# Kernel tuning notes

Measured on AMD Instinct MI355X. Metric: run time of the kernel, lower is better.

## Reference

```python
import jax, jax.numpy as jnp
import numpy as np

EPS = 1e-4

@jax.custom_vjp
def binarize(x):
    # BinaryConnectDeterministic: sign with sign(0)=+1
    return jnp.where(x >= 0, 1.0, -1.0).astype(x.dtype)

def _bin_fwd(x):
    return binarize(x), x

def _bin_bwd(x, g):
    # straight-through estimator, clipped to |x| <= 1
    return (g * (jnp.abs(x) <= 1).astype(g.dtype),)

binarize.defvjp(_bin_fwd, _bin_bwd)

def ap2(x):
    # approximate power-of-2: sign(x) * 2^round(log2|x|); grad is 0 a.e. (round/sign)
    a = jnp.maximum(jnp.abs(x), 1e-38)
    return jnp.sign(x) * jnp.exp2(jnp.round(jnp.log2(a)))

def shift_bn(x, gamma, beta, axes):
    # shift-based batch norm (BNN paper): var approximated via centered*AP2(centered),
    # inverse std and gamma replaced by their AP2 approximations. Training-mode batch stats.
    mean = jnp.mean(x, axis=axes, keepdims=True)
    c = x - mean
    var = jnp.mean(c * ap2(c), axis=axes, keepdims=True)
    xhat = c * ap2(1.0 / jnp.sqrt(var + EPS))
    shape = [1] * x.ndim
    shape[1] = x.shape[1]
    return ap2(gamma.reshape(shape)) * xhat + beta.reshape(shape)

def conv_bin(x, w, b):
    y = jax.lax.conv_general_dilated(x, binarize(w), (1, 1), [(1, 1), (1, 1)],
                                     dimension_numbers=('NCHW', 'OIHW', 'NCHW'))
    return y + b[None, :, None, None]

def maxpool3s2(x):
    return jax.lax.reduce_window(x, -jnp.inf, jax.lax.max,
                                 (1, 1, 3, 3), (1, 1, 2, 2), 'VALID')


def setup_inputs() -> dict:
    key = jax.random.key(0)
    ks = jax.random.split(key, 8)
    B, NU = 2048, 2048
    inp = {
        'x': jax.random.normal(ks[0], (B, 784), jnp.float32),
        'conv1_w': jax.random.normal(ks[1], (32, 1, 3, 3), jnp.float32) * 0.1,
        'conv1_b': jnp.zeros((32,), jnp.float32),
        'g1': jnp.ones((32,), jnp.float32), 'b1': jnp.zeros((32,), jnp.float32),
        'conv2_w': jax.random.normal(ks[2], (64, 32, 3, 3), jnp.float32) * 0.1,
        'conv2_b': jnp.zeros((64,), jnp.float32),
        'g2': jnp.ones((64,), jnp.float32), 'b2': jnp.zeros((64,), jnp.float32),
        'lin3_w': jax.random.normal(ks[3], (NU, 10816), jnp.float32) * 0.02,
        'lin3_b': jnp.zeros((NU,), jnp.float32),
        'g3': jnp.ones((NU,), jnp.float32), 'b3': jnp.zeros((NU,), jnp.float32),
        'lin4_w': jax.random.normal(ks[4], (10, NU), jnp.float32) * 0.02,
        'lin4_b': jnp.zeros((10,), jnp.float32),
    }
    return inp


def reference(x, conv1_w, conv1_b, g1, b1, conv2_w, conv2_b, g2, b2,
              lin3_w, lin3_b, g3, b3, lin4_w, lin4_b):
    h = x.reshape(-1, 1, 28, 28)
    h = jax.nn.relu(conv_bin(h, conv1_w, conv1_b))
    h = shift_bn(h, g1, b1, axes=(0, 2, 3))
    h = binarize(h)
    h = jax.nn.relu(conv_bin(h, conv2_w, conv2_b))
    h = maxpool3s2(h)                       # [B,64,13,13]
    h = shift_bn(h, g2, b2, axes=(0, 2, 3))
    h = binarize(h)
    h = h.reshape(h.shape[0], -1)           # [B,10816]
    h = jax.nn.relu(h @ binarize(lin3_w).T + lin3_b)
    h = shift_bn(h, g3, b3, axes=(0,))
    h = binarize(h)
    return h @ binarize(lin4_w).T + lin4_b  # [B,10] (no norm4/logsoftmax in forward)
```

## Files before the change

### kernel.cpp

```cpp
#include <hip/hip_runtime.h>

#define BB 2048
#define IMG 784
#define HWD 28
#define C1 32
#define C2 64
#define PP 169
#define PD 13
#define F3 10816
#define N3 2048
#define K4W 32
#define NOUT 10
#define CONV 27
#define PADW 30
#define OCCHUNK 8
#define IMGC 29
#define SCRP 740

typedef unsigned long long u64;
typedef int v4i __attribute__((ext_vector_type(4)));
typedef int v16i __attribute__((ext_vector_type(16)));

#define GLOAD16(gp, lp) __builtin_amdgcn_global_load_lds( \
    (__attribute__((address_space(1))) void*)(gp),        \
    (__attribute__((address_space(3))) void*)(lp), 16, 0, 0)

__device__ __forceinline__ float ap2mag(float c) {
    unsigned int a = __float_as_uint(c) & 0x7fffffffu;
    unsigned int e = (a >> 23) + ((a & 0x7fffffu) > 0x3504f3u);
    return __uint_as_float(e << 23);
}
__device__ __forceinline__ float ap2sgn(float g) {
    unsigned int u = __float_as_uint(g);
    unsigned int a = u & 0x7fffffffu;
    if (a == 0) return 0.f;
    unsigned int e = (a >> 23) + ((a & 0x7fffffu) > 0x3504f3u);
    return __uint_as_float((u & 0x80000000u) | (e << 23));
}

__global__ __launch_bounds__(256) void stage0(const float* __restrict__ x,
                                              const float* __restrict__ w1, const float* __restrict__ cb1,
                                              float* __restrict__ part1, float* __restrict__ w1b,
                                              const float* __restrict__ w2, char* __restrict__ w2i8,
                                              const float* __restrict__ w3, char* __restrict__ wp3i,
                                              const float* __restrict__ w4, u64* __restrict__ wp4) {
    __shared__ float xs[30 * PADW];
    __shared__ float red[4 * C1];
    int n = blockIdx.x, tid = threadIdx.x;
    int lane = tid & 63, wv = tid >> 6;
    {
        int idx = n * 256 + tid;
        int nthr = gridDim.x * 256;
        int total = (N3 * F3) / 4;
        for (int t = idx; t < total; t += nthr) {
            float4 wv4 = *(const float4*)(w3 + (size_t)t * 4);
            unsigned int w = (wv4.x >= 0.f ? 0x01u : 0xffu)
                           | (wv4.y >= 0.f ? 0x01u : 0xffu) << 8
                           | (wv4.z >= 0.f ? 0x01u : 0xffu) << 16
                           | (wv4.w >= 0.f ? 0x01u : 0xffu) << 24;
            *(unsigned int*)(wp3i + (size_t)t * 4) = w;
        }
    }
    if (n == 0) {
        for (int i = tid; i < C1 * 9; i += 256) w1b[i] = (w1[i] >= 0.f) ? 1.f : -1.f;
    } else if (n == 1) {
        for (int i = tid; i < 2 * 9 * 64 * 16; i += 256) {
            int hf = i / 9216;
            int r = i - hf * 9216;
            int t = r >> 10;
            int l = (r >> 4) & 63;
            int j = i & 15;
            int oc = hf * 32 + (l & 31);
            int ic = ((l >> 5) << 4) + j;
            w2i8[i] = (w2[oc * 288 + ic * 9 + t] >= 0.f) ? (char)1 : (char)(-1);
        }
    } else if (n == 2) {
        for (int w = wv; w < NOUT * K4W; w += 4) {
            int o = w / K4W, j = w % K4W;
            float wvl = w4[o * N3 + j * 64 + lane];
            u64 mask = __ballot(wvl >= 0.f);
            if (lane == 0) wp4[w] = mask;
        }
    }
    for (int i = tid; i < 30 * PADW; i += 256) {
        int r = i / PADW - 1, c = i % PADW - 1;
        float v = 0.f;
        if (r >= 0 && r < HWD && c >= 0 && c < HWD) v = x[n * IMG + r * HWD + c];
        xs[i] = v;
    }
    __syncthreads();
    bool act = tid < 196;
    int r = tid / 7, c0 = (tid % 7) * 4;
    float win[18];
#pragma unroll
    for (int k = 0; k < 18; k++) win[k] = 0.f;
    if (act) {
#pragma unroll
        for (int ry = 0; ry < 3; ry++)
#pragma unroll
            for (int cx = 0; cx < 6; cx++)
                win[ry * 6 + cx] = xs[(r + ry) * PADW + c0 + cx];
    }
#pragma unroll
    for (int ch = 0; ch < C1; ch++) {
        float a = 0.f;
        if (act) {
            float k0 = (w1[ch * 9 + 0] >= 0.f) ? 1.f : -1.f, k1 = (w1[ch * 9 + 1] >= 0.f) ? 1.f : -1.f;
            float k2 = (w1[ch * 9 + 2] >= 0.f) ? 1.f : -1.f, k3 = (w1[ch * 9 + 3] >= 0.f) ? 1.f : -1.f;
            float k4 = (w1[ch * 9 + 4] >= 0.f) ? 1.f : -1.f, k5 = (w1[ch * 9 + 5] >= 0.f) ? 1.f : -1.f;
            float k6 = (w1[ch * 9 + 6] >= 0.f) ? 1.f : -1.f, k7 = (w1[ch * 9 + 7] >= 0.f) ? 1.f : -1.f;
            float k8 = (w1[ch * 9 + 8] >= 0.f) ? 1.f : -1.f;
            float b = cb1[ch];
#pragma unroll
            for (int px = 0; px < 4; px++) {
                float s = win[px] * k0 + win[px + 1] * k1 + win[px + 2] * k2
                        + win[6 + px] * k3 + win[7 + px] * k4 + win[8 + px] * k5
                        + win[12 + px] * k6 + win[13 + px] * k7 + win[14 + px] * k8;
                a += fmaxf(s + b, 0.f);
            }
        }
        for (int off = 32; off; off >>= 1) a += __shfl_down(a, off);
        if (lane == 0) red[wv * C1 + ch] = a;
    }
    __syncthreads();
    if (tid < C1) part1[n * C1 + tid] = red[tid] + red[C1 + tid] + red[2 * C1 + tid] + red[3 * C1 + tid];
}

__global__ __launch_bounds__(256) void conv1_var(const float* __restrict__ x,
                            const float* __restrict__ w1b,
                            const float* __restrict__ cb1, const float* __restrict__ mean1,
                            float* __restrict__ part) {
    __shared__ float xs[30 * PADW];
    __shared__ float red[4 * C1];
    int n = blockIdx.x, tid = threadIdx.x;
    for (int i = tid; i < 30 * PADW; i += 256) {
        int r = i / PADW - 1, c = i % PADW - 1;
        float v = 0.f;
        if (r >= 0 && r < HWD && c >= 0 && c < HWD) v = x[n * IMG + r * HWD + c];
        xs[i] = v;
    }
    __syncthreads();
    bool act = tid < 196;
    int r = tid / 7, c0 = (tid % 7) * 4;
    float win[18];
#pragma unroll
    for (int k = 0; k < 18; k++) win[k] = 0.f;
    if (act) {
#pragma unroll
        for (int ry = 0; ry < 3; ry++)
#pragma unroll
            for (int cx = 0; cx < 6; cx++)
                win[ry * 6 + cx] = xs[(r + ry) * PADW + c0 + cx];
    }
    int lane = tid & 63, wv = tid >> 6;
#pragma unroll
    for (int ch = 0; ch < C1; ch++) {
        float a = 0.f;
        if (act) {
            float k0 = w1b[ch * 9 + 0], k1 = w1b[ch * 9 + 1], k2 = w1b[ch * 9 + 2];
            float k3 = w1b[ch * 9 + 3], k4 = w1b[ch * 9 + 4], k5 = w1b[ch * 9 + 5];
            float k6 = w1b[ch * 9 + 6], k7 = w1b[ch * 9 + 7], k8 = w1b[ch * 9 + 8];
            float b = cb1[ch], m = mean1[ch];
#pragma unroll
            for (int px = 0; px < 4; px++) {
                float s = win[px] * k0 + win[px + 1] * k1 + win[px + 2] * k2
                        + win[6 + px] * k3 + win[7 + px] * k4 + win[8 + px] * k5
                        + win[12 + px] * k6 + win[13 + px] * k7 + win[14 + px] * k8;
                float v = fmaxf(s + b, 0.f);
                float c = v - m;
                a += fabsf(c) * ap2mag(c);
            }
        }
        for (int off = 32; off; off >>= 1) a += __shfl_down(a, off);
        if (lane == 0) red[wv * C1 + ch] = a;
    }
    __syncthreads();
    if (tid < C1) part[n * C1 + tid] = red[tid] + red[C1 + tid] + red[2 * C1 + tid] + red[3 * C1 + tid];
}

__global__ __launch_bounds__(256) void conv1_pack(const float* __restrict__ x,
                           const float* __restrict__ w1b,
                           const float* __restrict__ cb1, const float* __restrict__ mean1,
                           const float* __restrict__ scale1, const float* __restrict__ beta1,
                           unsigned int* __restrict__ s1p) {
    __shared__ float xs[30 * PADW];
    int n = blockIdx.x, tid = threadIdx.x;
    for (int i = tid; i < 30 * PADW; i += 256) {
        int r = i / PADW - 1, c = i % PADW - 1;
        float v = 0.f;
        if (r >= 0 && r < HWD && c >= 0 && c < HWD) v = x[n * IMG + r * HWD + c];
        xs[i] = v;
    }
    __syncthreads();
    if (tid >= 196) return;
    int r = tid / 7, c0 = (tid % 7) * 4;
    float win[18];
#pragma unroll
    for (int ry = 0; ry < 3; ry++)
#pragma unroll
        for (int cx = 0; cx < 6; cx++)
            win[ry * 6 + cx] = xs[(r + ry) * PADW + c0 + cx];
    unsigned int bits0 = 0, bits1 = 0, bits2 = 0, bits3 = 0;
#pragma unroll
    for (int ch = 0; ch < C1; ch++) {
        float k0 = w1b[ch * 9 + 0], k1 = w1b[ch * 9 + 1], k2 = w1b[ch * 9 + 2];
        float k3 = w1b[ch * 9 + 3], k4 = w1b[ch * 9 + 4], k5 = w1b[ch * 9 + 5];
        float k6 = w1b[ch * 9 + 6], k7 = w1b[ch * 9 + 7], k8 = w1b[ch * 9 + 8];
        float b = cb1[ch], m = mean1[ch], sc = scale1[ch], bt = beta1[ch];
#pragma unroll
        for (int px = 0; px < 4; px++) {
            float s = win[px] * k0 + win[px + 1] * k1 + win[px + 2] * k2
                    + win[6 + px] * k3 + win[7 + px] * k4 + win[8 + px] * k5
                    + win[12 + px] * k6 + win[13 + px] * k7 + win[14 + px] * k8;
            float v = fmaxf(s + b, 0.f);
            float val = sc * (v - m) + bt;
            unsigned int bit = (val >= 0.f ? 1u : 0u) << ch;
            if (px == 0) bits0 |= bit;
            else if (px == 1) bits1 |= bit;
            else if (px == 2) bits2 |= bit;
            else bits3 |= bit;
        }
    }
    uint4 w4v = make_uint4(bits0, bits1, bits2, bits3);
    *reinterpret_cast<uint4*>(&s1p[n * IMG + r * HWD + c0]) = w4v;
}

__global__ __launch_bounds__(256) void conv2pool(const unsigned int* __restrict__ s1p,
                                                 const char* __restrict__ w2i8,
                                                 const float* __restrict__ cb2,
                                                 short* __restrict__ p2i,
                                                 float* __restrict__ part2) {
    __shared__ char img[IMGC * IMGC * 32];
    __shared__ short scr[32 * SCRP];
    __shared__ float psum[OCCHUNK * PP];
    __shared__ float pm[C2];
    int n = blockIdx.x, tid = threadIdx.x;
    int lane = tid & 63, wv = tid >> 6;
    for (int i = tid; i < IMGC * IMGC; i += 256) {
        int r = i / IMGC, c = i - r * IMGC;
        unsigned int w = 0u;
        if (r >= 1 && c >= 1) w = s1p[n * IMG + (r - 1) * HWD + (c - 1)];
        unsigned int d[8];
        if (r == 0 || c == 0) {
#pragma unroll
            for (int e = 0; e < 8; e++) d[e] = 0u;
        } else {
#pragma unroll
            for (int e = 0; e < 8; e++) {
                unsigned int nib = (w >> (4 * e)) & 0xFu;
                unsigned int t = (nib & 1u) | ((nib & 2u) << 7) | ((nib & 4u) << 14) | ((nib & 8u) << 21);
                d[e] = 0xFFFFFFFFu - t * 0xFEu;
            }
        }
        *(uint4*)&img[i * 32] = make_uint4(d[0], d[1], d[2], d[3]);
        *(uint4*)&img[i * 32 + 16] = make_uint4(d[4], d[5], d[6], d[7]);
    }
    __syncthreads();
    int hh = lane >> 5;
    int l31 = lane & 31;
    for (int hf = 0; hf < 2; hf++) {
        v4i bf[9];
#pragma unroll
        for (int t = 0; t < 9; t++)
            bf[t] = *(const v4i*)(w2i8 + (hf * 9 + t) * 1024 + lane * 16);
#pragma unroll
        for (int j = 0; j < 3; j++) {
            int mtA = wv + 8 * j, mtB = mtA + 4;
            int pA = mtA * 32 + l31; if (pA > 728) pA = 728;
            int pB = mtB * 32 + l31; if (pB > 728) pB = 728;
            int yA = pA / 27, xA = pA - yA * 27;
            int yB = pB / 27, xB = pB - yB * 27;
            int aA = (yA * IMGC + xA) * 32 + hh * 16;
            int aB = (yB * IMGC + xB) * 32 + hh * 16;
            v16i accA = {0,0,0,0,0,0,0,0,0,0,0,0,0,0,0,0};
            v16i accB = {0,0,0,0,0,0,0,0,0,0,0,0,0,0,0,0};
#pragma unroll
            for (int ky = 0; ky < 3; ky++)
#pragma unroll
                for (int kx = 0; kx < 3; kx++) {
                    v4i fA = *(const v4i*)&img[aA + (ky * IMGC + kx) * 32];
                    v4i fB = *(const v4i*)&img[aB + (ky * IMGC + kx) * 32];
                    accA = __builtin_amdgcn_mfma_i32_32x32x32_i8(fA, bf[ky * 3 + kx], accA, 0, 0, 0);
                    accB = __builtin_amdgcn_mfma_i32_32x32x32_i8(fB, bf[ky * 3 + kx], accB, 0, 0, 0);
                }
            short* sr = &scr[l31 * SCRP];
#pragma unroll
            for (int g = 0; g < 4; g++) {
                short4 sA;
                sA.x = (short)accA[4 * g + 0]; sA.y = (short)accA[4 * g + 1];
                sA.z = (short)accA[4 * g + 2]; sA.w = (short)accA[4 * g + 3];
                *(short4*)&sr[mtA * 32 + g * 8 + 4 * hh] = sA;
            }
            if (mtB < 23) {
#pragma unroll
                for (int g = 0; g < 4; g++) {
                    short4 sB;
                    sB.x = (short)accB[4 * g + 0]; sB.y = (short)accB[4 * g + 1];
                    sB.z = (short)accB[4 * g + 2]; sB.w = (short)accB[4 * g + 3];
                    *(short4*)&sr[mtB * 32 + g * 8 + 4 * hh] = sB;
                }
            }
        }
        __syncthreads();
        for (int base = 0; base < 32; base += OCCHUNK) {
            for (int q = tid; q < OCCHUNK * PP; q += 256) {
                int ol = q / PP, pix = q - ol * PP;
                int py = pix / PD, px = pix - py * PD;
                const short* rr = &scr[(base + ol) * SCRP + (2 * py) * CONV + 2 * px];
                int m0 = max(max((int)rr[0], (int)rr[1]), (int)rr[2]);
                int m1 = max(max((int)rr[CONV], (int)rr[CONV + 1]), (int)rr[CONV + 2]);
                int m2 = max(max((int)rr[2 * CONV], (int)rr[2 * CONV + 1]), (int)rr[2 * CONV + 2]);
                int val = max(max(m0, m1), m2);
                int oc = hf * 32 + base + ol;
                p2i[n * F3 + oc * PP + pix] = (short)val;
                psum[q] = fmaxf((float)val + cb2[oc], 0.f);
            }
            __syncthreads();
            for (int ol = wv; ol < OCCHUNK; ol += 4) {
                float a = 0.f;
                for (int pp = lane; pp < PP; pp += 64) a += psum[ol * PP + pp];
                for (int off = 32; off; off >>= 1) a += __shfl_down(a, off);
                if (lane == 0) pm[hf * 32 + base + ol] = a;
            }
            __syncthreads();
        }
    }
    if (tid < C2) part2[n * C2 + tid] = pm[tid];
}

__global__ __launch_bounds__(256) void p2_var(const short* __restrict__ p2i,
                         const float* __restrict__ cb2,
                         const float* __restrict__ mean2, float* __restrict__ part) {
    int n = blockIdx.x, tid = threadIdx.x, lane = tid & 63, wv = tid >> 6;
    const short* rowb = p2i + (size_t)n * F3;
    __shared__ float red[C2];
#pragma unroll
    for (int i = 0; i < 16; i++) {
        int ch = wv * 16 + i;
        const short* row = rowb + ch * PP;
        float b = cb2[ch];
        float m = mean2[ch];
        float a = 0.f;
        for (int p = lane; p < PP; p += 64) {
            float v = fmaxf((float)row[p] + b, 0.f);
            float c = v - m;
            a += fabsf(c) * ap2mag(c);
        }
        for (int off = 32; off; off >>= 1) a += __shfl_down(a, off);
        if (lane == 0) red[ch] = a;
    }
    __syncthreads();
    if (tid < C2) part[n * C2 + tid] = red[tid];
}

__global__ __launch_bounds__(256) void reduce_stats(const float* __restrict__ part, int nch, int nblk,
                             const float* __restrict__ g, float* __restrict__ outv,
                             int mode, double count) {
    int ch = blockIdx.x, tid = threadIdx.x;
    double a = 0.0;
    for (int i = tid; i < nblk; i += 256) a += (double)part[(size_t)i * nch + ch];
    __shared__ double red[4];
    for (int off = 32; off; off >>= 1) a += __shfl_down(a, off);
    int lane = tid & 63, wv = tid >> 6;
    if (lane == 0) red[wv] = a;
    __syncthreads();
    if (tid == 0) {
        double s = red[0] + red[1] + red[2] + red[3];
        if (mode == 0) {
            outv[ch] = (float)(s / count);
        } else {
            float var = (float)(s / count);
            float inv = 1.0f / sqrtf(var + 1e-4f);
            outv[ch] = ap2sgn(g[ch]) * ap2mag(inv);
        }
    }
}

__global__ __launch_bounds__(256) void p2_packi8(const short* __restrict__ p2i, const float* __restrict__ cb2,
                        const float* __restrict__ mean2, const float* __restrict__ scale2,
                        const float* __restrict__ beta2, char* __restrict__ hp3i) {
    int idx = blockIdx.x * 256 + threadIdx.x;
    int nthr = gridDim.x * 256;
    int total = (BB * F3) / 4;
    for (int t = idx; t < total; t += nthr) {
        int base = t * 4;
        int f0 = base % F3;
        unsigned int w = 0;
#pragma unroll
        for (int e = 0; e < 4; e++) {
            int f = f0 + e;
            int oc = f / PP;
            float v = fmaxf((float)p2i[base + e] + cb2[oc], 0.f);
            float val = scale2[oc] * (v - mean2[oc]) + beta2[oc];
            w |= (val >= 0.f ? 0x01u : 0xffu) << (8 * e);
        }
        *(unsigned int*)(hp3i + base) = w;
    }
}

__global__ __launch_bounds__(256) void lin3_mfma(const char* __restrict__ hp3i,
                                                 const char* __restrict__ wp3i,
                                                 const float* __restrict__ b3l,
                                                 float* __restrict__ h3,
                                                 float* __restrict__ h3T,
                                                 float* __restrict__ part3) {
    __shared__ v4i aL[3][1024];
    __shared__ v4i bL[3][512];
    __shared__ float csr[4][32];
    int tid = threadIdx.x;
    int lane = tid & 63, wv = tid >> 6;
    int wr = wv >> 1, wc = wv & 1;
    int m0 = blockIdx.y * 128, n0 = blockIdx.x * 64;
    int loff = (lane & 15) * F3 + (lane >> 4) * 16;
    const char* gA0 = hp3i + (size_t)(m0 + wv * 16) * F3 + loff;
    const char* gA1 = gA0 + (size_t)64 * F3;
    const char* gB0 = wp3i + (size_t)(n0 + wv * 16) * F3 + loff;
    char* ldsA = (char*)&aL[0][0];
    char* ldsB = (char*)&bL[0][0];
    int sA = wv * 1024;
    v4i acc[4][2];
#pragma unroll
    for (int i = 0; i < 4; i++)
#pragma unroll
        for (int j = 0; j < 2; j++) acc[i][j] = (v4i){0, 0, 0, 0};

    auto stage = [&](int c) {
        int b = c % 3;
        const char* pA0 = gA0 + (size_t)c * 128;
        const char* pA1 = gA1 + (size_t)c * 128;
        const char* pB0 = gB0 + (size_t)c * 128;
        char* dA = ldsA + b * 16384 + sA;
        char* dB = ldsB + b * 8192 + sA;
        GLOAD16(pA0, dA);
        GLOAD16(pA1, dA + 4096);
        GLOAD16(pA0 + 64, dA + 8192);
        GLOAD16(pA1 + 64, dA + 12288);
        GLOAD16(pB0, dB);
        GLOAD16(pB0 + 64, dB + 4096);
    };
    auto compute = [&](int c, int nks) {
        int cur = c % 3;
        const v4i* aC = &aL[cur][0];
        const v4i* bC = &bL[cur][0];
        for (int ks = 0; ks < nks; ++ks) {
            v4i af[4], bf[2];
#pragma unroll
            for (int i = 0; i < 4; i++) af[i] = aC[ks * 512 + (wr * 4 + i) * 64 + lane];
#pragma unroll
            for (int j = 0; j < 2; j++) bf[j] = bC[ks * 256 + (wc * 2 + j) * 64 + lane];
            __builtin_amdgcn_s_setprio(1);
#pragma unroll
            for (int i = 0; i < 4; i++)
#pragma unroll
                for (int j = 0; j < 2; j++)
                    acc[i][j] = __builtin_amdgcn_mfma_i32_16x16x64_i8(af[i], bf[j], acc[i][j], 0, 0, 0);
            __builtin_amdgcn_s_setprio(0);
        }
    };

    stage(0);
    stage(1);
    asm volatile("s_waitcnt vmcnt(6)" ::: "memory");
    __builtin_amdgcn_s_barrier();
    __builtin_amdgcn_sched_barrier(0);
    for (int c = 0; c < 83; ++c) {
        stage(c + 2);
        compute(c, 2);
        asm volatile("s_waitcnt vmcnt(6)" ::: "memory");
        __builtin_amdgcn_s_barrier();
        __builtin_amdgcn_sched_barrier(0);
    }
    compute(83, 2);
    asm volatile("s_waitcnt vmcnt(0)" ::: "memory");
    __builtin_amdgcn_s_barrier();
    __builtin_amdgcn_sched_barrier(0);
    compute(84, 1);

    int q = lane >> 4, m16 = lane & 15;
    float cs[2] = {0.f, 0.f};
#pragma unroll
    for (int j = 0; j < 2; j++) {
        int col = n0 + wc * 32 + j * 16 + m16;
        float bias = b3l[col];
#pragma unroll
        for (int i = 0; i < 4; i++) {
            int rowb = m0 + wr * 64 + i * 16 + q * 4;
            float4 t4;
#pragma unroll
            for (int rg = 0; rg < 4; rg++) {
                float v = fmaxf((float)acc[i][j][rg] + bias, 0.f);
                h3[(size_t)(rowb + rg) * N3 + col] = v;
                ((float*)&t4)[rg] = v;
                cs[j] += v;
            }
            *(float4*)&h3T[(size_t)col * BB + rowb] = t4;
        }
    }
#pragma unroll
    for (int j = 0; j < 2; j++) {
        cs[j] += __shfl_xor(cs[j], 16);
        cs[j] += __shfl_xor(cs[j], 32);
        if (lane < 16) csr[wv][j * 16 + m16] = cs[j];
    }
    __syncthreads();
    if (tid < 64) {
        int wcc = tid >> 5, cc = tid & 31;
        part3[(size_t)blockIdx.y * N3 + n0 + tid] = csr[wcc][cc] + csr[2 + wcc][cc];
    }
}

__global__ __launch_bounds__(256) void h3_finish(const float* __restrict__ h3T,
                                                 const float* __restrict__ part3,
                                                 const float* __restrict__ g3,
                                                 float* __restrict__ mean3, float* __restrict__ scale3) {
    int nn = blockIdx.x, tid = threadIdx.x;
    __shared__ float msh;
    __shared__ double redd[4];
    if (tid < 64) {
        float a = (tid < 16) ? part3[(size_t)tid * N3 + nn] : 0.f;
        for (int off = 8; off; off >>= 1) a += __shfl_down(a, off);
        if (tid == 0) { float m = a / (float)BB; mean3[nn] = m; msh = m; }
    }
    __syncthreads();
    float m = msh;
    float acc = 0.f;
#pragma unroll
    for (int q = 0; q < 8; q++) {
        float v = h3T[(size_t)nn * BB + q * 256 + tid];
        float c = v - m;
        acc += fabsf(c) * ap2mag(c);
    }
    double a = (double)acc;
    for (int off = 32; off; off >>= 1) a += __shfl_down(a, off);
    int lane = tid & 63, wv = tid >> 6;
    if (lane == 0) redd[wv] = a;
    __syncthreads();
    if (tid == 0) {
        float var = (float)((redd[0] + redd[1] + redd[2] + redd[3]) / (double)BB);
        float inv = 1.0f / sqrtf(var + 1e-4f);
        scale3[nn] = ap2sgn(g3[nn]) * ap2mag(inv);
    }
}

__global__ __launch_bounds__(256) void h4_out(const float* __restrict__ h3,
                                              const float* __restrict__ mean3, const float* __restrict__ scale3,
                                              const float* __restrict__ bt3,
                                              const u64* __restrict__ wp4, const float* __restrict__ b4,
                                              float* __restrict__ out) {
    __shared__ u64 hb[K4W];
    __shared__ u64 wsh[NOUT * 33];
    int m = blockIdx.x, tid = threadIdx.x, lane = tid & 63, wv = tid >> 6;
    for (int i = tid; i < NOUT * K4W; i += 256) wsh[(i / K4W) * 33 + (i % K4W)] = wp4[i];
#pragma unroll
    for (int q = 0; q < 8; q++) {
        int j = wv * 8 + q;
        int f = j * 64 + lane;
        float v = h3[(size_t)m * N3 + f];
        float val = scale3[f] * (v - mean3[f]) + bt3[f];
        u64 mask = __ballot(val >= 0.f);
        if (lane == 0) hb[j] = mask;
    }
    __syncthreads();
    if (tid < NOUT) {
        int c = 0;
#pragma unroll
        for (int k = 0; k < K4W; k++) c += (int)__popcll(hb[k] ^ wsh[tid * 33 + k]);
        out[m * NOUT + tid] = (float)(N3 - 2 * c) + b4[tid];
    }
}

extern "C" void kernel_launch(void* const* d_in, const int* in_sizes, int n_in,
                              void* d_out, int out_size, void* d_ws, size_t ws_size,
                              hipStream_t stream) {
    const float* x   = (const float*)d_in[0];
    const float* w1  = (const float*)d_in[1];
    const float* cb1 = (const float*)d_in[2];
    const float* g1  = (const float*)d_in[3];
    const float* bt1 = (const float*)d_in[4];
    const float* w2  = (const float*)d_in[5];
    const float* cb2 = (const float*)d_in[6];
    const float* g2  = (const float*)d_in[7];
    const float* bt2 = (const float*)d_in[8];
    const float* w3  = (const float*)d_in[9];
    const float* b3l = (const float*)d_in[10];
    const float* g3  = (const float*)d_in[11];
    const float* bt3 = (const float*)d_in[12];
    const float* w4  = (const float*)d_in[13];
    const float* b4l = (const float*)d_in[14];
    float* out = (float*)d_out;

    char* base = (char*)d_ws;
    size_t off = 0;
    auto carve = [&](size_t bytes) { char* p = base + off; off = (off + bytes + 255) & ~(size_t)255; return p; };
    char* bufA = carve((size_t)BB * C2 * PP * 2);
    char* bufB = carve((size_t)BB * F3);
    char* bufC = carve((size_t)N3 * F3);
    short* p2i         = (short*)bufA;
    float* h3          = (float*)bufA;
    float* h3T         = (float*)(bufA + (size_t)BB * N3 * 4);
    char* hp3i         = bufB;
    unsigned int* s1p  = (unsigned int*)bufB;
    char* wp3i         = bufC;
    u64* wp4           = (u64*)carve((size_t)NOUT * K4W * 8);
    char* w2i8         = (char*)carve((size_t)2 * 9 * 64 * 16);
    float* w1b         = (float*)carve((size_t)C1 * 9 * 4);
    float* part1       = (float*)carve((size_t)BB * C1 * 4);
    float* part2       = (float*)carve((size_t)BB * C2 * 4);
    float* part3       = (float*)carve((size_t)16 * N3 * 4);
    float* fstats      = (float*)carve((size_t)(32 + 32 + 64 + 64 + 2048 + 2048) * 4);
    float* mean1 = fstats;          float* scale1 = fstats + 32;
    float* mean2 = fstats + 64;     float* scale2 = fstats + 128;
    float* mean3 = fstats + 192;    float* scale3 = fstats + 2240;

    stage0<<<BB, 256, 0, stream>>>(x, w1, cb1, part1, w1b, w2, w2i8, w3, wp3i, w4, wp4);
    reduce_stats<<<C1, 256, 0, stream>>>(part1, C1, BB, g1, mean1, 0, (double)BB * IMG);
    conv1_var<<<BB, 256, 0, stream>>>(x, w1b, cb1, mean1, part1);
    reduce_stats<<<C1, 256, 0, stream>>>(part1, C1, BB, g1, scale1, 1, (double)BB * IMG);
    conv1_pack<<<BB, 256, 0, stream>>>(x, w1b, cb1, mean1, scale1, bt1, s1p);
    conv2pool<<<BB, 256, 0, stream>>>(s1p, w2i8, cb2, p2i, part2);
    reduce_stats<<<C2, 256, 0, stream>>>(part2, C2, BB, g2, mean2, 0, (double)BB * PP);
    p2_var<<<BB, 256, 0, stream>>>(p2i, cb2, mean2, part2);
    reduce_stats<<<C2, 256, 0, stream>>>(part2, C2, BB, g2, scale2, 1, (double)BB * PP);
    p2_packi8<<<2048, 256, 0, stream>>>(p2i, cb2, mean2, scale2, bt2, hp3i);
    lin3_mfma<<<dim3(32, 16), 256, 0, stream>>>(hp3i, wp3i, b3l, h3, h3T, part3);
    h3_finish<<<N3, 256, 0, stream>>>(h3T, part3, g3, mean3, scale3);
    h4_out<<<BB, 256, 0, stream>>>(h3, mean3, scale3, bt3, wp4, b4l, out);

    (void)in_sizes; (void)n_in; (void)out_size; (void)ws_size;
}
```

Measured before the change: 549.3 us.

## Restructure lin3 int8 GEMM into single-wave 64x64 tiles with 4-stage barrier-free pipeline

The binarized lin3 GEMM kernel now runs one wavefront per block, each computing a 64x64 output tile with 4x4 MFMA accumulators instead of a 4-wave 128x64 block. Its K loop uses a 4-deep LDS ring of 64-byte chunks synchronised only by vmcnt waits, with no block barriers. The goal is to drop the cross-wave barrier stalls and raise per-wave MFMA density. In exchange, each block's operand reuse is lower, giving more global traffic per FLOP, and the column partial sums double to 32 rows, which h3_finish now reduces in pairs.

```diff
diff --git a/kernel.cpp b/kernel.cpp
--- a/kernel.cpp
+++ b/kernel.cpp
@@ -398,93 +398,80 @@
     }
 }
 
-__global__ __launch_bounds__(256) void lin3_mfma(const char* __restrict__ hp3i,
-                                                 const char* __restrict__ wp3i,
-                                                 const float* __restrict__ b3l,
-                                                 float* __restrict__ h3,
-                                                 float* __restrict__ h3T,
-                                                 float* __restrict__ part3) {
-    __shared__ v4i aL[3][1024];
-    __shared__ v4i bL[3][512];
-    __shared__ float csr[4][32];
-    int tid = threadIdx.x;
-    int lane = tid & 63, wv = tid >> 6;
-    int wr = wv >> 1, wc = wv & 1;
-    int m0 = blockIdx.y * 128, n0 = blockIdx.x * 64;
+__global__ __launch_bounds__(64) void lin3_mfma(const char* __restrict__ hp3i,
+                                                const char* __restrict__ wp3i,
+                                                const float* __restrict__ b3l,
+                                                float* __restrict__ h3,
+                                                float* __restrict__ h3T,
+                                                float* __restrict__ part3) {
+    __shared__ v4i lds[2048];
+    int lane = threadIdx.x;
+    int m0 = blockIdx.y * 64, n0 = blockIdx.x * 64;
     int loff = (lane & 15) * F3 + (lane >> 4) * 16;
-    const char* gA0 = hp3i + (size_t)(m0 + wv * 16) * F3 + loff;
-    const char* gA1 = gA0 + (size_t)64 * F3;
-    const char* gB0 = wp3i + (size_t)(n0 + wv * 16) * F3 + loff;
-    char* ldsA = (char*)&aL[0][0];
-    char* ldsB = (char*)&bL[0][0];
-    int sA = wv * 1024;
-    v4i acc[4][2];
+    const char* gA = hp3i + (size_t)m0 * F3 + loff;
+    const char* gB = wp3i + (size_t)n0 * F3 + loff;
+    char* ldsc = (char*)&lds[0];
+    v4i acc[4][4];
 #pragma unroll
     for (int i = 0; i < 4; i++)
 #pragma unroll
-        for (int j = 0; j < 2; j++) acc[i][j] = (v4i){0, 0, 0, 0};
+        for (int j = 0; j < 4; j++) acc[i][j] = (v4i){0, 0, 0, 0};
 
     auto stage = [&](int c) {
-        int b = c % 3;
-        const char* pA0 = gA0 + (size_t)c * 128;
-        const char* pA1 = gA1 + (size_t)c * 128;
-        const char* pB0 = gB0 + (size_t)c * 128;
-        char* dA = ldsA + b * 16384 + sA;
-        char* dB = ldsB + b * 8192 + sA;
-        GLOAD16(pA0, dA);
-        GLOAD16(pA1, dA + 4096);
-        GLOAD16(pA0 + 64, dA + 8192);
-        GLOAD16(pA1 + 64, dA + 12288);
-        GLOAD16(pB0, dB);
-        GLOAD16(pB0 + 64, dB + 4096);
+        int b = c & 3;
+        const char* pA = gA + (size_t)c * 64;
+        const char* pB = gB + (size_t)c * 64;
+        char* dA = ldsc + b * 8192;
+        char* dB = dA + 4096;
+        GLOAD16(pA,            dA);
+        GLOAD16(pA + 16 * F3,  dA + 1024);
+        GLOAD16(pA + 32 * F3,  dA + 2048);
+        GLOAD16(pA + 48 * F3,  dA + 3072);
+        GLOAD16(pB,            dB);
+        GLOAD16(pB + 16 * F3,  dB + 1024);
+        GLOAD16(pB + 32 * F3,  dB + 2048);
+        GLOAD16(pB + 48 * F3,  dB + 3072);
     };
-    auto compute = [&](int c, int nks) {
-        int cur = c % 3;
-        const v4i* aC = &aL[cur][0];
-        const v4i* bC = &bL[cur][0];
-        for (int ks = 0; ks < nks; ++ks) {
-            v4i af[4], bf[2];
-#pragma unroll
-            for (int i = 0; i < 4; i++) af[i] = aC[ks * 512 + (wr * 4 + i) * 64 + lane];
-#pragma unroll
-            for (int j = 0; j < 2; j++) bf[j] = bC[ks * 256 + (wc * 2 + j) * 64 + lane];
-            __builtin_amdgcn_s_setprio(1);
-#pragma unroll
-            for (int i = 0; i < 4; i++)
-#pragma unroll
-                for (int j = 0; j < 2; j++)
-                    acc[i][j] = __builtin_amdgcn_mfma_i32_16x16x64_i8(af[i], bf[j], acc[i][j], 0, 0, 0);
-            __builtin_amdgcn_s_setprio(0);
-        }
+    auto compute = [&](int c) {
+        int b = c & 3;
+        const v4i* L = &lds[b * 512];
+        v4i af[4], bf[4];
+#pragma unroll
+        for (int i = 0; i < 4; i++) af[i] = L[i * 64 + lane];
+#pragma unroll
+        for (int j = 0; j < 4; j++) bf[j] = L[256 + j * 64 + lane];
+        __builtin_amdgcn_s_setprio(1);
+#pragma unroll
+        for (int i = 0; i < 4; i++)
+#pragma unroll
+            for (int j = 0; j < 4; j++)
+                acc[i][j] = __builtin_amdgcn_mfma_i32_16x16x64_i8(af[i], bf[j], acc[i][j], 0, 0, 0);
+        __builtin_amdgcn_s_setprio(0);
     };
 
-    stage(0);
-    stage(1);
-    asm volatile("s_waitcnt vmcnt(6)" ::: "memory");
-    __builtin_amdgcn_s_barrier();
-    __builtin_amdgcn_sched_barrier(0);
-    for (int c = 0; c < 83; ++c) {
-        stage(c + 2);
-        compute(c, 2);
-        asm volatile("s_waitcnt vmcnt(6)" ::: "memory");
-        __builtin_amdgcn_s_barrier();
-        __builtin_amdgcn_sched_barrier(0);
-    }
-    compute(83, 2);
+    stage(0); stage(1); stage(2);
+    for (int c = 0; c < 166; ++c) {
+        stage(c + 3);
+        asm volatile("s_waitcnt vmcnt(24)" ::: "memory");
+        compute(c);
+    }
+    asm volatile("s_waitcnt vmcnt(16)" ::: "memory");
+    compute(166);
+    asm volatile("s_waitcnt vmcnt(8)" ::: "memory");
+    compute(167);
     asm volatile("s_waitcnt vmcnt(0)" ::: "memory");
-    __builtin_amdgcn_s_barrier();
-    __builtin_amdgcn_sched_barrier(0);
-    compute(84, 1);
+    compute(168);
 
     int q = lane >> 4, m16 = lane & 15;
-    float cs[2] = {0.f, 0.f};
-#pragma unroll
-    for (int j = 0; j < 2; j++) {
-        int col = n0 + wc * 32 + j * 16 + m16;
+    float cs[4];
+#pragma unroll
+    for (int j = 0; j < 4; j++) {
+        cs[j] = 0.f;
+        int col = n0 + j * 16 + m16;
         float bias = b3l[col];
 #pragma unroll
         for (int i = 0; i < 4; i++) {
-            int rowb = m0 + wr * 64 + i * 16 + q * 4;
+            int rowb = m0 + i * 16 + q * 4;
             float4 t4;
 #pragma unroll
             for (int rg = 0; rg < 4; rg++) {
@@ -495,17 +482,13 @@
             }
             *(float4*)&h3T[(size_t)col * BB + rowb] = t4;
         }
-    }
-#pragma unroll
-    for (int j = 0; j < 2; j++) {
         cs[j] += __shfl_xor(cs[j], 16);
         cs[j] += __shfl_xor(cs[j], 32);
-        if (lane < 16) csr[wv][j * 16 + m16] = cs[j];
-    }
-    __syncthreads();
-    if (tid < 64) {
-        int wcc = tid >> 5, cc = tid & 31;
-        part3[(size_t)blockIdx.y * N3 + n0 + tid] = csr[wcc][cc] + csr[2 + wcc][cc];
+    }
+    if (lane < 16) {
+#pragma unroll
+        for (int j = 0; j < 4; j++)
+            part3[(size_t)blockIdx.y * N3 + n0 + j * 16 + lane] = cs[j];
     }
 }
 
@@ -517,7 +500,8 @@
     __shared__ float msh;
     __shared__ double redd[4];
     if (tid < 64) {
-        float a = (tid < 16) ? part3[(size_t)tid * N3 + nn] : 0.f;
+        float a = 0.f;
+        if (tid < 16) a = part3[(size_t)(2 * tid) * N3 + nn] + part3[(size_t)(2 * tid + 1) * N3 + nn];
         for (int off = 8; off; off >>= 1) a += __shfl_down(a, off);
         if (tid == 0) { float m = a / (float)BB; mean3[nn] = m; msh = m; }
     }
@@ -606,7 +590,7 @@
     float* w1b         = (float*)carve((size_t)C1 * 9 * 4);
     float* part1       = (float*)carve((size_t)BB * C1 * 4);
     float* part2       = (float*)carve((size_t)BB * C2 * 4);
-    float* part3       = (float*)carve((size_t)16 * N3 * 4);
+    float* part3       = (float*)carve((size_t)32 * N3 * 4);
     float* fstats      = (float*)carve((size_t)(32 + 32 + 64 + 64 + 2048 + 2048) * 4);
     float* mean1 = fstats;          float* scale1 = fstats + 32;
     float* mean2 = fstats + 64;     float* scale2 = fstats + 128;
@@ -622,7 +606,7 @@
     p2_var<<<BB, 256, 0, stream>>>(p2i, cb2, mean2, part2);
     reduce_stats<<<C2, 256, 0, stream>>>(part2, C2, BB, g2, scale2, 1, (double)BB * PP);
     p2_packi8<<<2048, 256, 0, stream>>>(p2i, cb2, mean2, scale2, bt2, hp3i);
-    lin3_mfma<<<dim3(32, 16), 256, 0, stream>>>(hp3i, wp3i, b3l, h3, h3T, part3);
+    lin3_mfma<<<dim3(32, 32), 64, 0, stream>>>(hp3i, wp3i, b3l, h3, h3T, part3);
     h3_finish<<<N3, 256, 0, stream>>>(h3T, part3, g3, mean3, scale3);
     h4_out<<<BB, 256, 0, stream>>>(h3, mean3, scale3, bt3, wp4, b4l, out);
 
```

New measurement: 576.9 us. +5.0%, slower.

## Enlarge lin3 GEMM block tile to 128x128 with 8 waves

Applied to the files above, without the earlier changes.

The int8 MFMA GEMM for the 10816-wide linear layer now uses 512-thread blocks covering a 128x128 output tile instead of 256 threads on 128x64. The grid halves to 16x16 blocks and each wave issues fewer global-to-LDS loads per stage. This raises reuse of the A operand across more output columns and cuts global traffic for activations. In exchange the kernel uses more LDS per block and launches only 256 blocks, which may underfill the GPU's compute units.

```diff
diff --git a/kernel.cpp b/kernel.cpp
--- a/kernel.cpp
+++ b/kernel.cpp
@@ -398,26 +398,22 @@
     }
 }
 
-__global__ __launch_bounds__(256) void lin3_mfma(const char* __restrict__ hp3i,
+__global__ __launch_bounds__(512) void lin3_mfma(const char* __restrict__ hp3i,
                                                  const char* __restrict__ wp3i,
                                                  const float* __restrict__ b3l,
                                                  float* __restrict__ h3,
                                                  float* __restrict__ h3T,
                                                  float* __restrict__ part3) {
     __shared__ v4i aL[3][1024];
-    __shared__ v4i bL[3][512];
-    __shared__ float csr[4][32];
+    __shared__ v4i bL[3][1024];
+    __shared__ float csr[8][32];
     int tid = threadIdx.x;
     int lane = tid & 63, wv = tid >> 6;
-    int wr = wv >> 1, wc = wv & 1;
-    int m0 = blockIdx.y * 128, n0 = blockIdx.x * 64;
+    int wr = wv >> 2, wc = wv & 3;
+    int m0 = blockIdx.y * 128, n0 = blockIdx.x * 128;
     int loff = (lane & 15) * F3 + (lane >> 4) * 16;
-    const char* gA0 = hp3i + (size_t)(m0 + wv * 16) * F3 + loff;
-    const char* gA1 = gA0 + (size_t)64 * F3;
-    const char* gB0 = wp3i + (size_t)(n0 + wv * 16) * F3 + loff;
-    char* ldsA = (char*)&aL[0][0];
-    char* ldsB = (char*)&bL[0][0];
-    int sA = wv * 1024;
+    const char* gA = hp3i + (size_t)(m0 + wv * 16) * F3 + loff;
+    const char* gB = wp3i + (size_t)(n0 + wv * 16) * F3 + loff;
     v4i acc[4][2];
 #pragma unroll
     for (int i = 0; i < 4; i++)
@@ -426,28 +422,23 @@
 
     auto stage = [&](int c) {
         int b = c % 3;
-        const char* pA0 = gA0 + (size_t)c * 128;
-        const char* pA1 = gA1 + (size_t)c * 128;
-        const char* pB0 = gB0 + (size_t)c * 128;
-        char* dA = ldsA + b * 16384 + sA;
-        char* dB = ldsB + b * 8192 + sA;
-        GLOAD16(pA0, dA);
-        GLOAD16(pA1, dA + 4096);
-        GLOAD16(pA0 + 64, dA + 8192);
-        GLOAD16(pA1 + 64, dA + 12288);
-        GLOAD16(pB0, dB);
-        GLOAD16(pB0 + 64, dB + 4096);
+        const char* pA = gA + (size_t)c * 128;
+        const char* pB = gB + (size_t)c * 128;
+        char* dA = (char*)&aL[b][0] + wv * 1024;
+        char* dB = (char*)&bL[b][0] + wv * 1024;
+        GLOAD16(pA,      dA);
+        GLOAD16(pA + 64, dA + 8192);
+        GLOAD16(pB,      dB);
+        GLOAD16(pB + 64, dB + 8192);
     };
     auto compute = [&](int c, int nks) {
-        int cur = c % 3;
-        const v4i* aC = &aL[cur][0];
-        const v4i* bC = &bL[cur][0];
+        int b = c % 3;
         for (int ks = 0; ks < nks; ++ks) {
             v4i af[4], bf[2];
 #pragma unroll
-            for (int i = 0; i < 4; i++) af[i] = aC[ks * 512 + (wr * 4 + i) * 64 + lane];
-#pragma unroll
-            for (int j = 0; j < 2; j++) bf[j] = bC[ks * 256 + (wc * 2 + j) * 64 + lane];
+            for (int i = 0; i < 4; i++) af[i] = aL[b][ks * 512 + (wr * 4 + i) * 64 + lane];
+#pragma unroll
+            for (int j = 0; j < 2; j++) bf[j] = bL[b][ks * 512 + (wc * 2 + j) * 64 + lane];
             __builtin_amdgcn_s_setprio(1);
 #pragma unroll
             for (int i = 0; i < 4; i++)
@@ -458,15 +449,14 @@
         }
     };
 
-    stage(0);
-    stage(1);
-    asm volatile("s_waitcnt vmcnt(6)" ::: "memory");
+    stage(0); stage(1);
+    asm volatile("s_waitcnt vmcnt(4)" ::: "memory");
     __builtin_amdgcn_s_barrier();
     __builtin_amdgcn_sched_barrier(0);
     for (int c = 0; c < 83; ++c) {
         stage(c + 2);
         compute(c, 2);
-        asm volatile("s_waitcnt vmcnt(6)" ::: "memory");
+        asm volatile("s_waitcnt vmcnt(4)" ::: "memory");
         __builtin_amdgcn_s_barrier();
         __builtin_amdgcn_sched_barrier(0);
     }
@@ -503,9 +493,9 @@
         if (lane < 16) csr[wv][j * 16 + m16] = cs[j];
     }
     __syncthreads();
-    if (tid < 64) {
-        int wcc = tid >> 5, cc = tid & 31;
-        part3[(size_t)blockIdx.y * N3 + n0 + tid] = csr[wcc][cc] + csr[2 + wcc][cc];
+    if (tid < 128) {
+        int wcg = tid >> 5, cc = tid & 31;
+        part3[(size_t)blockIdx.y * N3 + n0 + tid] = csr[wcg][cc] + csr[4 + wcg][cc];
     }
 }
 
@@ -622,7 +612,7 @@
     p2_var<<<BB, 256, 0, stream>>>(p2i, cb2, mean2, part2);
     reduce_stats<<<C2, 256, 0, stream>>>(part2, C2, BB, g2, scale2, 1, (double)BB * PP);
     p2_packi8<<<2048, 256, 0, stream>>>(p2i, cb2, mean2, scale2, bt2, hp3i);
-    lin3_mfma<<<dim3(32, 16), 256, 0, stream>>>(hp3i, wp3i, b3l, h3, h3T, part3);
+    lin3_mfma<<<dim3(16, 16), 512, 0, stream>>>(hp3i, wp3i, b3l, h3, h3T, part3);
     h3_finish<<<N3, 256, 0, stream>>>(h3T, part3, g3, mean3, scale3);
     h4_out<<<BB, 256, 0, stream>>>(h3, mean3, scale3, bt3, wp4, b4l, out);
 
```

After: 557.9 us. Within noise of the previous version (+1.6%).
